# Kernel tuning notes

Measured on AMD Instinct MI355X. Metric: run time of the kernel, lower is better.

Reference implementation:

```python
import jax, jax.numpy as jnp
import numpy as np
from jax import lax

VOCAB = 32000
EMB = 512
HID = 1024
BATCH = 64
MAX_LEN = 30
STEPS = MAX_LEN + 2
SOS = 1
PAD = 0


def setup_inputs() -> dict:
    key = jax.random.key(0)
    ks = jax.random.split(key, 9)
    s = 0.05
    target = jax.random.randint(ks[0], (BATCH, 1), 0, VOCAB)
    encoder_hidden = jax.random.normal(ks[1], (1, BATCH, HID), dtype=jnp.float32)
    emb = jax.random.normal(ks[2], (VOCAB, EMB), dtype=jnp.float32) * s
    emb = emb.at[PAD].set(0.0)  # padding_idx row zeroed like torch
    W_ih = jax.random.normal(ks[3], (3 * HID, EMB), dtype=jnp.float32) * s
    W_hh = jax.random.normal(ks[4], (3 * HID, HID), dtype=jnp.float32) * s
    b_ih = jax.random.normal(ks[5], (3 * HID,), dtype=jnp.float32) * s
    b_hh = jax.random.normal(ks[6], (3 * HID,), dtype=jnp.float32) * s
    fc_W = jax.random.normal(ks[7], (VOCAB, HID), dtype=jnp.float32) * s
    fc_b = jax.random.normal(ks[8], (VOCAB,), dtype=jnp.float32) * s
    return {"target": target, "encoder_hidden": encoder_hidden, "emb": emb,
            "W_ih": W_ih, "W_hh": W_hh, "b_ih": b_ih, "b_hh": b_hh,
            "fc_W": fc_W, "fc_b": fc_b}


def reference(target, encoder_hidden, emb, W_ih, W_hh, b_ih, b_hh, fc_W, fc_b):
    B = target.shape[0]

    def step(carry, _):
        tok, h = carry                      # tok [B] int, h [B,H]
        x = emb[tok]                        # [B,E] embedding lookup
        gi = x @ W_ih.T + b_ih              # [B,3H]
        gh = h @ W_hh.T + b_hh              # [B,3H]
        i_r, i_z, i_n = jnp.split(gi, 3, axis=-1)
        h_r, h_z, h_n = jnp.split(gh, 3, axis=-1)
        r = jax.nn.sigmoid(i_r + h_r)
        z = jax.nn.sigmoid(i_z + h_z)
        n = jnp.tanh(i_n + r * h_n)
        h_new = (1.0 - z) * n + z * h       # torch GRU update
        logits = h_new @ fc_W.T + fc_b      # [B,V]
        logp = jax.nn.log_softmax(logits, axis=-1)
        tok_new = jnp.argmax(logp, axis=-1)  # greedy feedback (topk, k=1)
        return (tok_new, h_new), logp

    h0 = encoder_hidden[0]                  # num_layers == 1
    tok0 = jnp.full((B,), SOS, dtype=jnp.int32)
    (_, hT), outs = lax.scan(step, (tok0, h0), None, length=STEPS)
    decoder_outputs = jnp.transpose(outs, (1, 0, 2))  # [B, STEPS, V]
    return decoder_outputs, hT[None]
```

## Files before the change

kernel.cpp:

```cpp
#include <hip/hip_runtime.h>

#define VV 32000
#define EE 512
#define HH 1024
#define NB 64
#define NSTEP 32

typedef __attribute__((ext_vector_type(8))) short short8;
typedef __attribute__((ext_vector_type(4))) float f32x4;
typedef unsigned long long u64;

#define MFMA16(a, b, c) __builtin_amdgcn_mfma_f32_16x16x32_bf16((a), (b), (c), 0, 0, 0)

__device__ __forceinline__ unsigned short f2bf(float f) {
  unsigned int u = __float_as_uint(f);
  u += 0x7fffu + ((u >> 16) & 1u);
  return (unsigned short)(u >> 16);
}
__device__ __forceinline__ float bf2f(unsigned short b) {
  return __uint_as_float(((unsigned int)b) << 16);
}
__device__ __forceinline__ float sigmoidf_(float x) { return 1.0f / (1.0f + expf(-x)); }
__device__ __forceinline__ unsigned int ordkey(float f) {
  unsigned int u = __float_as_uint(f);
  return u ^ ((u >> 31) ? 0xFFFFFFFFu : 0x80000000u);
}
__device__ __forceinline__ float ordkey_inv(unsigned int u) {
  return __uint_as_float((u & 0x80000000u) ? (u ^ 0x80000000u) : ~u);
}

__global__ __launch_bounds__(256) void prep_wcat(const float* __restrict__ Wih,
                                                 const float* __restrict__ Whh,
                                                 unsigned short* __restrict__ wm,
                                                 unsigned short* __restrict__ wr) {
  int ub = blockIdx.x / 3, g = blockIdx.x % 3;
  for (int e = threadIdx.x; e < 48 * 512; e += 256) {
    int ks = e >> 9, lane = (e >> 3) & 63, j = e & 7;
    int row = g * HH + ub * 16 + (lane & 15);
    int k = ks * 32 + ((lane >> 4) << 3) + j;
    float f = (k < EE) ? Wih[(size_t)row * EE + k] : Whh[(size_t)row * HH + (k - EE)];
    unsigned short m_ = f2bf(f);
    size_t idx = (((size_t)(ub * 3 + g) * 48 + ks) * 64 + lane) * 8 + j;
    wm[idx] = m_;
    wr[idx] = f2bf(f - bf2f(m_));
  }
}

__global__ __launch_bounds__(256) void prep_wfc(const float* __restrict__ fcW,
                                                unsigned short* __restrict__ wfc) {
  int vg = blockIdx.x;
  for (int e = threadIdx.x; e < 32768; e += 256) {
    int ks = e >> 10, n = (e >> 9) & 1, lane = (e >> 3) & 63, j = e & 7;
    int v = vg * 32 + n * 16 + (lane & 15);
    int k = ks * 32 + ((lane >> 4) << 3) + j;
    wfc[(((size_t)vg * 32 + ks) * 2 + n) * 512 + lane * 8 + j] = f2bf(fcW[(size_t)v * HH + k]);
  }
}

__global__ __launch_bounds__(256) void init_kernel(
    const float* __restrict__ enc, const float* __restrict__ emb, float* __restrict__ h4a,
    unsigned short* __restrict__ ham, unsigned short* __restrict__ har,
    unsigned short* __restrict__ xam, unsigned short* __restrict__ xar,
    int* __restrict__ cnt, int* __restrict__ arrive) {
  int i = blockIdx.x * 256 + threadIdx.x;
  int b = i >> 10, u = i & 1023;
  float hv = enc[i];
  h4a[i] = hv;
  unsigned short m_ = f2bf(hv);
  size_t idx = (((size_t)(b >> 4) * 32 + (u >> 5)) * 64 + ((b & 15) + (((u >> 3) & 3) << 4))) * 8 + (u & 7);
  ham[idx] = m_;
  har[idx] = f2bf(hv - bf2f(m_));
  if (i < NB * EE) {
    int b2 = i >> 9, k = i & 511;
    float xv = emb[EE + k];
    unsigned short xm = f2bf(xv);
    size_t xi = (((size_t)(b2 >> 4) * 16 + (k >> 5)) * 64 + ((b2 & 15) + (((k >> 3) & 3) << 4))) * 8 + (k & 7);
    xam[xi] = xm;
    xar[xi] = f2bf(xv - bf2f(xm));
  }
  if (i < NB) { cnt[i] = 0; arrive[i] = 0; }
}

__device__ __forceinline__ void gru_body(
    int bid, int tid, float (*red)[16][65],
    const unsigned short* xam, const unsigned short* xar,
    const unsigned short* him, const unsigned short* hir,
    const float* h4in, float* h4out,
    const unsigned short* wm, const unsigned short* wrs,
    const float* bih, const float* bhh,
    unsigned short* hom, unsigned short* hor) {
  const int lane = tid & 63, w = tid >> 6;
  const int ub = bid >> 2, mg = bid & 3;
  f32x4 aR{}, aZ{}, aNX{}, aNH{};
  const short8* XM = (const short8*)xam;
  const short8* XR = (const short8*)xar;
  const short8* HM = (const short8*)him;
  const short8* HR = (const short8*)hir;
  const short8* WM = (const short8*)wm;
  const short8* WR = (const short8*)wrs;
#pragma unroll
  for (int s = 0; s < 12; ++s) {
    int ks = w * 12 + s;
    short8 am, ar;
    if (ks < 16) {
      int o = (mg * 16 + ks) * 64 + lane;
      am = XM[o]; ar = XR[o];
    } else {
      int o = (mg * 32 + (ks - 16)) * 64 + lane;
      am = HM[o]; ar = HR[o];
    }
    {
      int o = ((ub * 3 + 0) * 48 + ks) * 64 + lane;
      short8 wmv = WM[o], wrv = WR[o];
      aR = MFMA16(am, wmv, aR); aR = MFMA16(ar, wmv, aR); aR = MFMA16(am, wrv, aR);
    }
    {
      int o = ((ub * 3 + 1) * 48 + ks) * 64 + lane;
      short8 wmv = WM[o], wrv = WR[o];
      aZ = MFMA16(am, wmv, aZ); aZ = MFMA16(ar, wmv, aZ); aZ = MFMA16(am, wrv, aZ);
    }
    {
      int o = ((ub * 3 + 2) * 48 + ks) * 64 + lane;
      short8 wmv = WM[o], wrv = WR[o];
      if (ks < 16) {
        aNX = MFMA16(am, wmv, aNX); aNX = MFMA16(ar, wmv, aNX); aNX = MFMA16(am, wrv, aNX);
      } else {
        aNH = MFMA16(am, wmv, aNH); aNH = MFMA16(ar, wmv, aNH); aNH = MFMA16(am, wrv, aNH);
      }
    }
  }
#pragma unroll
  for (int reg = 0; reg < 4; ++reg) {
    int rr = ((lane >> 4) << 2) + reg, c = lane & 15;
    red[w][rr][c] = aR[reg];
    red[w][rr][16 + c] = aZ[reg];
    red[w][rr][32 + c] = aNX[reg];
    red[w][rr][48 + c] = aNH[reg];
  }
  __syncthreads();
  const int mrow = tid >> 4, uu = tid & 15;
  float R = 0.f, Z = 0.f, NX = 0.f, NH = 0.f;
#pragma unroll
  for (int q = 0; q < 4; ++q) {
    R += red[q][mrow][uu];
    Z += red[q][mrow][16 + uu];
    NX += red[q][mrow][32 + uu];
    NH += red[q][mrow][48 + uu];
  }
  const int b = mg * 16 + mrow, u = ub * 16 + uu;
  float r = sigmoidf_(R + bih[u] + bhh[u]);
  float z = sigmoidf_(Z + bih[HH + u] + bhh[HH + u]);
  float n = tanhf(NX + bih[2 * HH + u] + r * (NH + bhh[2 * HH + u]));
  float hold = h4in[b * HH + u];
  float hn = (1.0f - z) * n + z * hold;
  h4out[b * HH + u] = hn;
  unsigned short m_ = f2bf(hn);
  size_t idx = (((size_t)(b >> 4) * 32 + (u >> 5)) * 64 + ((b & 15) + (((u >> 3) & 3) << 4))) * 8 + (u & 7);
  hom[idx] = m_;
  hor[idx] = f2bf(hn - bf2f(m_));
}

__global__ __launch_bounds__(256, 4) void gru_kernel(
    const unsigned short* xam, const unsigned short* xar,
    const unsigned short* him, const unsigned short* hir,
    const float* h4in, float* h4out,
    const unsigned short* wm, const unsigned short* wrs,
    const float* bih, const float* bhh,
    unsigned short* hom, unsigned short* hor) {
  __shared__ float red[4][16][65];
  gru_body(blockIdx.x, threadIdx.x, red, xam, xar, him, hir, h4in, h4out, wm, wrs, bih, bhh, hom, hor);
}

__global__ __launch_bounds__(256, 8) void fc_kernel(
    const unsigned short* __restrict__ ham,
    const unsigned short* __restrict__ wfc, const float* __restrict__ fcb,
    unsigned short* __restrict__ lgb, u64* __restrict__ blkkeys, int t) {
  const int tid = threadIdx.x;
  const int lane = tid & 63, w = tid >> 6;
  const int vg = blockIdx.x;
  f32x4 acc0{}, acc1{};
  const short8* HM = (const short8*)ham + (size_t)w * 2048;
  const short8* W = (const short8*)wfc + (size_t)vg * 4096;
#pragma unroll 8
  for (int ks = 0; ks < 32; ++ks) {
    short8 am = HM[ks * 64 + lane];
    short8 w0 = W[(ks * 2 + 0) * 64 + lane];
    short8 w1 = W[(ks * 2 + 1) * 64 + lane];
    acc0 = MFMA16(am, w0, acc0);
    acc1 = MFMA16(am, w1, acc1);
  }
  const int r0 = lane >> 4, c0 = lane & 15;
  const float b0 = fcb[vg * 32 + c0];
  const float b1 = fcb[vg * 32 + 16 + c0];
  u64 kk[4];
#pragma unroll
  for (int reg = 0; reg < 4; ++reg) {
    const int b = w * 16 + r0 * 4 + reg;
    float v0 = acc0[reg] + b0;
    float v1 = acc1[reg] + b1;
    size_t ro = ((size_t)b * NSTEP + t) * VV + (size_t)vg * 32 + c0;
    lgb[ro] = f2bf(v0);
    lgb[ro + 16] = f2bf(v1);
    u64 k0 = ((u64)ordkey(v0) << 32) | (u64)(0xFFFFFFFFu - (unsigned)(vg * 32 + c0));
    u64 k1 = ((u64)ordkey(v1) << 32) | (u64)(0xFFFFFFFFu - (unsigned)(vg * 32 + 16 + c0));
    kk[reg] = k0 > k1 ? k0 : k1;
  }
#pragma unroll
  for (int d = 1; d < 16; d <<= 1)
#pragma unroll
    for (int reg = 0; reg < 4; ++reg) {
      u64 o = __shfl_xor(kk[reg], d, 64);
      if (o > kk[reg]) kk[reg] = o;
    }
  if (c0 == 0) {
#pragma unroll
    for (int reg = 0; reg < 4; ++reg)
      blkkeys[(size_t)(w * 16 + r0 * 4 + reg) * 1000 + vg] = kk[reg];
  }
}

__global__ __launch_bounds__(256) void sel_kernel(
    const unsigned short* __restrict__ lgb, const u64* __restrict__ blkkeys,
    int* __restrict__ cnt, int* __restrict__ cand, int* __restrict__ arrive,
    const float* __restrict__ fcW, const float* __restrict__ fcb,
    const float* __restrict__ emb, const float* __restrict__ h4,
    unsigned short* __restrict__ xam, unsigned short* __restrict__ xar, int t) {
  const int b = blockIdx.x >> 3, q = blockIdx.x & 7;
  const int tid = threadIdx.x;
  __shared__ u64 skey[256];
  __shared__ int slast, stok;
  __shared__ u64 rkey[256];

  const u64* kb = blkkeys + (size_t)b * 1000;
  u64 mk = 0;
  for (int i = tid; i < 1000; i += 256) {
    u64 k = kb[i];
    if (k > mk) mk = k;
  }
  skey[tid] = mk;
  __syncthreads();
  for (int off = 128; off > 0; off >>= 1) {
    if (tid < off && skey[tid + off] > skey[tid]) skey[tid] = skey[tid + off];
    __syncthreads();
  }
  const float Mf = ordkey_inv((unsigned)(skey[0] >> 32));
  const float thr = Mf - 0.10f;

  const short8* r8v = (const short8*)(lgb + ((size_t)b * NSTEP + t) * VV);
  for (int i = q * 500 + tid; i < (q + 1) * 500; i += 256) {
    short8 v8 = r8v[i];
#pragma unroll
    for (int e = 0; e < 8; ++e) {
      float x = bf2f((unsigned short)v8[e]);
      if (x >= thr) {
        int p = atomicAdd(&cnt[b], 1);
        if (p < 256) atomicExch(&cand[b * 256 + p], i * 8 + e);
      }
    }
  }
  __syncthreads();
  if (tid == 0) slast = (atomicAdd(&arrive[b], 1) == 7) ? 1 : 0;
  __syncthreads();
  if (!slast) return;

  int n = atomicAdd(&cnt[b], 0);
  if (n > 256) n = 256;
  const int w = tid >> 6, ln = tid & 63;
  for (int ci = w; ci < n; ci += 4) {
    int v = atomicAdd(&cand[b * 256 + ci], 0);
    float p = 0.f;
#pragma unroll
    for (int qq = 0; qq < 16; ++qq)
      p += h4[b * HH + ln + (qq << 6)] * fcW[(size_t)v * HH + ln + (qq << 6)];
#pragma unroll
    for (int d = 1; d < 64; d <<= 1) p += __shfl_xor(p, d);
    if (ln == 0)
      rkey[ci] = ((u64)ordkey(p + fcb[v]) << 32) | (u64)(0xFFFFFFFFu - (unsigned)v);
  }
  __syncthreads();
  if (tid == 0) {
    u64 bk = 0;
    for (int ci = 0; ci < n; ++ci)
      if (rkey[ci] > bk) bk = rkey[ci];
    stok = (int)(0xFFFFFFFFu - (unsigned)(bk & 0xFFFFFFFFu));
    atomicExch(&cnt[b], 0);
    atomicExch(&arrive[b], 0);
  }
  __syncthreads();

  const int tok = stok;
  for (int k = tid; k < EE; k += 256) {
    float xv = emb[(size_t)tok * EE + k];
    unsigned short xm = f2bf(xv);
    size_t xi = (((size_t)(b >> 4) * 16 + (k >> 5)) * 64 + ((b & 15) + (((k >> 3) & 3) << 4))) * 8 + (k & 7);
    xam[xi] = xm;
    xar[xi] = f2bf(xv - bf2f(xm));
  }
}

__global__ __launch_bounds__(256) void lsm_kernel(const unsigned short* __restrict__ lgb,
                                                  const float* __restrict__ h4,
                                                  float* __restrict__ out) {
  const int bid = blockIdx.x;
  const int tid = threadIdx.x;
  if (bid >= 2048) {
    int i = (bid - 2048) * 256 + tid;
    out[(size_t)NB * NSTEP * VV + i] = h4[i];
    return;
  }
  const short8* r8v = (const short8*)(lgb + (size_t)bid * VV);
  float* orow = out + (size_t)bid * VV;
  __shared__ float mred[256], sred[256];
  float m = -INFINITY, s = 0.f;
  for (int i = tid; i < VV / 8; i += 256) {
    short8 v8 = r8v[i];
#pragma unroll
    for (int c = 0; c < 8; ++c) {
      float x = bf2f((unsigned short)v8[c]);
      if (x > m) { s = s * expf(m - x) + 1.0f; m = x; }
      else s += expf(x - m);
    }
  }
  mred[tid] = m; sred[tid] = s;
  __syncthreads();
  for (int off = 128; off > 0; off >>= 1) {
    if (tid < off) {
      float m1 = mred[tid], s1 = sred[tid];
      float m2 = mred[tid + off], s2 = sred[tid + off];
      float M = fmaxf(m1, m2);
      mred[tid] = M;
      sred[tid] = s1 * expf(m1 - M) + s2 * expf(m2 - M);
    }
    __syncthreads();
  }
  const float lse = mred[0] + logf(sred[0]);
  for (int i = tid; i < VV / 8; i += 256) {
    short8 v8 = r8v[i];
    float4 o0, o1;
    o0.x = bf2f((unsigned short)v8[0]) - lse;
    o0.y = bf2f((unsigned short)v8[1]) - lse;
    o0.z = bf2f((unsigned short)v8[2]) - lse;
    o0.w = bf2f((unsigned short)v8[3]) - lse;
    o1.x = bf2f((unsigned short)v8[4]) - lse;
    o1.y = bf2f((unsigned short)v8[5]) - lse;
    o1.z = bf2f((unsigned short)v8[6]) - lse;
    o1.w = bf2f((unsigned short)v8[7]) - lse;
    ((float4*)orow)[i * 2] = o0;
    ((float4*)orow)[i * 2 + 1] = o1;
  }
}

extern "C" void kernel_launch(void* const* d_in, const int* in_sizes, int n_in,
                              void* d_out, int out_size, void* d_ws, size_t ws_size,
                              hipStream_t stream) {
  const float* enc = (const float*)d_in[1];
  const float* emb = (const float*)d_in[2];
  const float* Wih = (const float*)d_in[3];
  const float* Whh = (const float*)d_in[4];
  const float* bih = (const float*)d_in[5];
  const float* bhh = (const float*)d_in[6];
  const float* fcW = (const float*)d_in[7];
  const float* fcb = (const float*)d_in[8];
  float* out = (float*)d_out;

  char* ws = (char*)d_ws;
  unsigned short* wfc = (unsigned short*)ws; ws += (size_t)32768000 * 2;
  unsigned short* wcm = (unsigned short*)ws; ws += (size_t)4718592 * 2;
  unsigned short* wcr = (unsigned short*)ws; ws += (size_t)4718592 * 2;
  unsigned short* hAm = (unsigned short*)ws; ws += (size_t)65536 * 2;
  unsigned short* hAr = (unsigned short*)ws; ws += (size_t)65536 * 2;
  unsigned short* hBm = (unsigned short*)ws; ws += (size_t)65536 * 2;
  unsigned short* hBr = (unsigned short*)ws; ws += (size_t)65536 * 2;
  unsigned short* xam = (unsigned short*)ws; ws += (size_t)32768 * 2;
  unsigned short* xar = (unsigned short*)ws; ws += (size_t)32768 * 2;
  float* h4a = (float*)ws; ws += (size_t)NB * HH * 4;
  float* h4b = (float*)ws; ws += (size_t)NB * HH * 4;
  u64* blkkeys = (u64*)ws; ws += (size_t)NB * 1000 * 8;
  int* cnt = (int*)ws; ws += (size_t)NB * 4;
  int* arrive = (int*)ws; ws += (size_t)NB * 4;
  int* cand = (int*)ws; ws += (size_t)NB * 256 * 4;
  unsigned short* lgb = (unsigned short*)ws; ws += (size_t)NB * NSTEP * VV * 2;

  prep_wfc<<<1000, 256, 0, stream>>>(fcW, wfc);
  prep_wcat<<<192, 256, 0, stream>>>(Wih, Whh, wcm, wcr);
  init_kernel<<<256, 256, 0, stream>>>(enc, emb, h4a, hAm, hAr, xam, xar, cnt, arrive);

  for (int t = 0; t < NSTEP; ++t) {
    const float* hin = (t & 1) ? h4b : h4a;
    float* hout = (t & 1) ? h4a : h4b;
    const unsigned short* him = (t & 1) ? hBm : hAm;
    const unsigned short* hir = (t & 1) ? hBr : hAr;
    unsigned short* hom = (t & 1) ? hAm : hBm;
    unsigned short* hor = (t & 1) ? hAr : hBr;
    gru_kernel<<<256, 256, 0, stream>>>(xam, xar, him, hir, hin, hout, wcm, wcr, bih, bhh, hom, hor);
    fc_kernel<<<1000, 256, 0, stream>>>(hom, wfc, fcb, lgb, blkkeys, t);
    sel_kernel<<<512, 256, 0, stream>>>(lgb, blkkeys, cnt, cand, arrive, fcW, fcb, emb, hout, xam, xar, t);
  }
  lsm_kernel<<<2304, 256, 0, stream>>>(lgb, h4a, out);
}
```

Baseline: 1.709 ms.

## Split GRU K-loop across 12 waves and vectorize weight prep kernels

The GRU step kernel now uses 768 threads (12 waves), each covering 4 K-slices instead of 12, with a larger shared-memory reduction across the 12 partial accumulators. The aim is to shorten the serial MFMA chain per wave and expose more memory-level parallelism in the latency-bound per-step GRU. Separately, the bf16 weight-prep kernels now read float4 pairs and write short8 vectors instead of scalar elements. The trade-off is a larger shared-memory reduction and fewer resident blocks per CU.

```diff
diff --git a/kernel.cpp b/kernel.cpp
--- a/kernel.cpp
+++ b/kernel.cpp
@@ -34,26 +34,43 @@
                                                  unsigned short* __restrict__ wm,
                                                  unsigned short* __restrict__ wr) {
   int ub = blockIdx.x / 3, g = blockIdx.x % 3;
-  for (int e = threadIdx.x; e < 48 * 512; e += 256) {
-    int ks = e >> 9, lane = (e >> 3) & 63, j = e & 7;
+  for (int e = threadIdx.x; e < 48 * 64; e += 256) {
+    int ks = e >> 6, lane = e & 63;
     int row = g * HH + ub * 16 + (lane & 15);
-    int k = ks * 32 + ((lane >> 4) << 3) + j;
-    float f = (k < EE) ? Wih[(size_t)row * EE + k] : Whh[(size_t)row * HH + (k - EE)];
-    unsigned short m_ = f2bf(f);
-    size_t idx = (((size_t)(ub * 3 + g) * 48 + ks) * 64 + lane) * 8 + j;
-    wm[idx] = m_;
-    wr[idx] = f2bf(f - bf2f(m_));
+    int k0 = ks * 32 + ((lane >> 4) << 3);
+    const float* srcp = (k0 < EE) ? (Wih + (size_t)row * EE + k0)
+                                  : (Whh + (size_t)row * HH + (k0 - EE));
+    float4 f0 = ((const float4*)srcp)[0];
+    float4 f1 = ((const float4*)srcp)[1];
+    float fs[8] = {f0.x, f0.y, f0.z, f0.w, f1.x, f1.y, f1.z, f1.w};
+    short8 om, orr;
+#pragma unroll
+    for (int j = 0; j < 8; ++j) {
+      unsigned short m_ = f2bf(fs[j]);
+      om[j] = (short)m_;
+      orr[j] = (short)f2bf(fs[j] - bf2f(m_));
+    }
+    size_t o8 = ((size_t)(ub * 3 + g) * 48 + ks) * 64 + lane;
+    ((short8*)wm)[o8] = om;
+    ((short8*)wr)[o8] = orr;
   }
 }
 
 __global__ __launch_bounds__(256) void prep_wfc(const float* __restrict__ fcW,
                                                 unsigned short* __restrict__ wfc) {
   int vg = blockIdx.x;
-  for (int e = threadIdx.x; e < 32768; e += 256) {
-    int ks = e >> 10, n = (e >> 9) & 1, lane = (e >> 3) & 63, j = e & 7;
+  for (int e = threadIdx.x; e < 4096; e += 256) {
+    int ks = e >> 7, n = (e >> 6) & 1, lane = e & 63;
     int v = vg * 32 + n * 16 + (lane & 15);
-    int k = ks * 32 + ((lane >> 4) << 3) + j;
-    wfc[(((size_t)vg * 32 + ks) * 2 + n) * 512 + lane * 8 + j] = f2bf(fcW[(size_t)v * HH + k]);
+    int k0 = ks * 32 + ((lane >> 4) << 3);
+    const float4* src = (const float4*)(fcW + (size_t)v * HH + k0);
+    float4 f0 = src[0];
+    float4 f1 = src[1];
+    float fs[8] = {f0.x, f0.y, f0.z, f0.w, f1.x, f1.y, f1.z, f1.w};
+    short8 o;
+#pragma unroll
+    for (int j = 0; j < 8; ++j) o[j] = (short)f2bf(fs[j]);
+    ((short8*)wfc)[(size_t)((vg * 32 + ks) * 2 + n) * 64 + lane] = o;
   }
 }
 
@@ -81,16 +98,16 @@
   if (i < NB) { cnt[i] = 0; arrive[i] = 0; }
 }
 
-__device__ __forceinline__ void gru_body(
-    int bid, int tid, float (*red)[16][65],
-    const unsigned short* xam, const unsigned short* xar,
-    const unsigned short* him, const unsigned short* hir,
-    const float* h4in, float* h4out,
-    const unsigned short* wm, const unsigned short* wrs,
-    const float* bih, const float* bhh,
-    unsigned short* hom, unsigned short* hor) {
-  const int lane = tid & 63, w = tid >> 6;
-  const int ub = bid >> 2, mg = bid & 3;
+__global__ __launch_bounds__(768, 3) void gru_kernel(
+    const unsigned short* __restrict__ xam, const unsigned short* __restrict__ xar,
+    const unsigned short* __restrict__ him, const unsigned short* __restrict__ hir,
+    const float* __restrict__ h4in, float* __restrict__ h4out,
+    const unsigned short* __restrict__ wm, const unsigned short* __restrict__ wrs,
+    const float* __restrict__ bih, const float* __restrict__ bhh,
+    unsigned short* __restrict__ hom, unsigned short* __restrict__ hor) {
+  __shared__ float red[12][16][65];
+  const int tid = threadIdx.x, lane = tid & 63, w = tid >> 6;
+  const int ub = blockIdx.x >> 2, mg = blockIdx.x & 3;
   f32x4 aR{}, aZ{}, aNX{}, aNH{};
   const short8* XM = (const short8*)xam;
   const short8* XR = (const short8*)xar;
@@ -99,8 +116,8 @@
   const short8* WM = (const short8*)wm;
   const short8* WR = (const short8*)wrs;
 #pragma unroll
-  for (int s = 0; s < 12; ++s) {
-    int ks = w * 12 + s;
+  for (int s = 0; s < 4; ++s) {
+    int ks = w * 4 + s;
     short8 am, ar;
     if (ks < 16) {
       int o = (mg * 16 + ks) * 64 + lane;
@@ -138,37 +155,28 @@
     red[w][rr][48 + c] = aNH[reg];
   }
   __syncthreads();
-  const int mrow = tid >> 4, uu = tid & 15;
-  float R = 0.f, Z = 0.f, NX = 0.f, NH = 0.f;
-#pragma unroll
-  for (int q = 0; q < 4; ++q) {
-    R += red[q][mrow][uu];
-    Z += red[q][mrow][16 + uu];
-    NX += red[q][mrow][32 + uu];
-    NH += red[q][mrow][48 + uu];
-  }
-  const int b = mg * 16 + mrow, u = ub * 16 + uu;
-  float r = sigmoidf_(R + bih[u] + bhh[u]);
-  float z = sigmoidf_(Z + bih[HH + u] + bhh[HH + u]);
-  float n = tanhf(NX + bih[2 * HH + u] + r * (NH + bhh[2 * HH + u]));
-  float hold = h4in[b * HH + u];
-  float hn = (1.0f - z) * n + z * hold;
-  h4out[b * HH + u] = hn;
-  unsigned short m_ = f2bf(hn);
-  size_t idx = (((size_t)(b >> 4) * 32 + (u >> 5)) * 64 + ((b & 15) + (((u >> 3) & 3) << 4))) * 8 + (u & 7);
-  hom[idx] = m_;
-  hor[idx] = f2bf(hn - bf2f(m_));
-}
-
-__global__ __launch_bounds__(256, 4) void gru_kernel(
-    const unsigned short* xam, const unsigned short* xar,
-    const unsigned short* him, const unsigned short* hir,
-    const float* h4in, float* h4out,
-    const unsigned short* wm, const unsigned short* wrs,
-    const float* bih, const float* bhh,
-    unsigned short* hom, unsigned short* hor) {
-  __shared__ float red[4][16][65];
-  gru_body(blockIdx.x, threadIdx.x, red, xam, xar, him, hir, h4in, h4out, wm, wrs, bih, bhh, hom, hor);
+  if (tid < 256) {
+    const int mrow = tid >> 4, uu = tid & 15;
+    float R = 0.f, Z = 0.f, NX = 0.f, NH = 0.f;
+#pragma unroll
+    for (int q = 0; q < 12; ++q) {
+      R += red[q][mrow][uu];
+      Z += red[q][mrow][16 + uu];
+      NX += red[q][mrow][32 + uu];
+      NH += red[q][mrow][48 + uu];
+    }
+    const int b = mg * 16 + mrow, u = ub * 16 + uu;
+    float r = sigmoidf_(R + bih[u] + bhh[u]);
+    float z = sigmoidf_(Z + bih[HH + u] + bhh[HH + u]);
+    float n = tanhf(NX + bih[2 * HH + u] + r * (NH + bhh[2 * HH + u]));
+    float hold = h4in[b * HH + u];
+    float hn = (1.0f - z) * n + z * hold;
+    h4out[b * HH + u] = hn;
+    unsigned short m_ = f2bf(hn);
+    size_t idx = (((size_t)(b >> 4) * 32 + (u >> 5)) * 64 + ((b & 15) + (((u >> 3) & 3) << 4))) * 8 + (u & 7);
+    hom[idx] = m_;
+    hor[idx] = f2bf(hn - bf2f(m_));
+  }
 }
 
 __global__ __launch_bounds__(256, 8) void fc_kernel(
@@ -392,7 +400,7 @@
     const unsigned short* hir = (t & 1) ? hBr : hAr;
     unsigned short* hom = (t & 1) ? hAm : hBm;
     unsigned short* hor = (t & 1) ? hAr : hBr;
-    gru_kernel<<<256, 256, 0, stream>>>(xam, xar, him, hir, hin, hout, wcm, wcr, bih, bhh, hom, hor);
+    gru_kernel<<<256, 768, 0, stream>>>(xam, xar, him, hir, hin, hout, wcm, wcr, bih, bhh, hom, hor);
     fc_kernel<<<1000, 256, 0, stream>>>(hom, wfc, fcb, lgb, blkkeys, t);
     sel_kernel<<<512, 256, 0, stream>>>(lgb, blkkeys, cnt, cand, arrive, fcW, fcb, emb, hout, xam, xar, t);
   }
```

Result: faster. 1.650 ms (median of 2 runs) (-3.4%).
